# Performance work log

Hardware: AMD Instinct MI355X
Metric: run time of the kernel (lower is better)

Reference implementation:

```python
import jax, jax.numpy as jnp
import numpy as np

N_LEAVES = 8192   # perfect binary tree, depth 13
SEQ = 4096        # sequenceSize
EMB = 100         # embedSize
NCLS = 2          # numClasses


def setup_inputs() -> dict:
    key = jax.random.key(0)
    k = jax.random.split(key, 7)
    return {
        "leaf_seqs": jax.random.normal(k[0], (N_LEAVES, SEQ), dtype=jnp.float32),
        # torch nn.Linear stores weight as [out, in]; y = x @ W.T + b
        "We": jax.random.normal(k[1], (EMB, SEQ), dtype=jnp.float32) / np.sqrt(SEQ).astype(np.float32),
        "be": jax.random.normal(k[2], (EMB,), dtype=jnp.float32) * 0.01,
        "W": jax.random.normal(k[3], (EMB, 2 * EMB), dtype=jnp.float32) / np.sqrt(2 * EMB).astype(np.float32),
        "b": jax.random.normal(k[4], (EMB,), dtype=jnp.float32) * 0.01,
        "Wp": jax.random.normal(k[5], (NCLS, EMB), dtype=jnp.float32) / np.sqrt(EMB).astype(np.float32),
        "bp": jax.random.normal(k[6], (NCLS,), dtype=jnp.float32) * 0.01,
    }


def reference(leaf_seqs, We, be, W, b, Wp, bp):
    # Level-order (tree-batched) evaluation of the recursive RNN over a
    # perfect binary tree. Leaves: relu(embedding(seq)); internal nodes:
    # relu(W @ cat(left, right)); root: projection -> class logits.
    h = jax.nn.relu(leaf_seqs @ We.T + be)              # [n_leaves, emb]
    depth = int(np.log2(N_LEAVES))
    for _ in range(depth):                               # fixed small loop over levels
        # adjacent siblings: reshape gives cat((left, right), dim=1) per pair
        pairs = h.reshape(h.shape[0] // 2, 2 * h.shape[1])  # [n/2, 2*emb]
        h = jax.nn.relu(pairs @ W.T + b)                 # [n/2, emb]
    logits = h @ Wp.T + bp                               # [1, numClasses]
    return logits
```

## Files before the change

### kernel.cpp

```cpp
#include <hip/hip_runtime.h>


typedef _Float16 half_t;
typedef __attribute__((ext_vector_type(8))) _Float16 half8;
typedef __attribute__((ext_vector_type(4))) float floatx4;

#define VMCNT_4 0xF74
#define VMCNT_0 0xF70

__device__ __forceinline__ void gld_lds16(const float* g, float* l) {
  __builtin_amdgcn_global_load_lds((const __attribute__((address_space(1))) void*)g,
                                   (__attribute__((address_space(3))) void*)l, 16, 0, 0);
}

__device__ __forceinline__ void cvt_hilo(const floatx4& a, const floatx4& b, half8& hi, half8& lo) {
#pragma unroll
  for (int j = 0; j < 4; ++j) {
    float v = a[j];
    half_t hh = (half_t)v;
    hi[j] = hh; lo[j] = (half_t)(v - (float)hh);
  }
#pragma unroll
  for (int j = 0; j < 4; ++j) {
    float v = b[j];
    half_t hh = (half_t)v;
    hi[4 + j] = hh; lo[4 + j] = (half_t)(v - (float)hh);
  }
}

__global__ __launch_bounds__(256) void bprep(const float* __restrict__ We,
                                             half_t* __restrict__ Bf) {
  int t = blockIdx.x * 256 + threadIdx.x;
  if (t >= 51200) return;
  int n = t >> 9;
  int kp = t & 511;
  int k0 = kp * 8;
  int ks = k0 >> 5;
  int q = (k0 >> 3) & 3;
  int c = n >> 4, m = n & 15;
  int lane = q * 16 + m;

  const float* src = We + (size_t)n * 4096 + k0;
  half8 hv, lv;
#pragma unroll
  for (int j = 0; j < 8; ++j) {
    float w = src[j];
    half_t hh = (half_t)w;
    hv[j] = hh; lv[j] = (half_t)(w - (float)hh);
  }
  size_t base = (size_t)(ks * 14 + c * 2) * 64 + lane;
  *(half8*)(Bf + base * 8) = hv;
  *(half8*)(Bf + (base + 64) * 8) = lv;
}

__global__ __launch_bounds__(64) void wprep(const float* __restrict__ W,
                                            half_t* __restrict__ Wf) {
  int ks = blockIdx.x / 7, tt = blockIdx.x % 7;
  int lane = threadIdx.x;
  int q = lane >> 4, n = lane & 15;
  int col = tt * 16 + n;
  int kb = ks * 32 + q * 8;
  half8 hv, lv;
#pragma unroll
  for (int j = 0; j < 8; ++j) {
    int k = kb + j;
    float w = (col < 100 && k < 200) ? W[(size_t)col * 200 + k] : 0.f;
    half_t hh = (half_t)w;
    hv[j] = hh; lv[j] = (half_t)(w - (float)hh);
  }
  size_t base = (size_t)(ks * 14 + tt * 2) * 64 + lane;
  *(half8*)(Wf + base * 8) = hv;
  *(half8*)(Wf + (base + 64) * 8) = lv;
}

__global__ __launch_bounds__(512, 1) void leaf_mfma(const float* __restrict__ A,
                                                    const half8* __restrict__ Bf,
                                                    const float* __restrict__ be,
                                                    float* __restrict__ h0) {
  __shared__ __align__(16) float lds[3 * 8320];
  const int tid = threadIdx.x;
  const int lane = tid & 63;
  const int wave = tid >> 6;
  const int q = lane >> 4, m = lane & 15;
  const int r0 = blockIdx.x * 32;

  floatx4 acc[2][7];
#pragma unroll
  for (int t = 0; t < 2; ++t)
#pragma unroll
    for (int c = 0; c < 7; ++c) acc[t][c] = (floatx4){0.f, 0.f, 0.f, 0.f};

  const float* gbase = A + (size_t)(r0 + wave * 4) * 4096 + lane * 4;
  const int ldso = (wave * 4) * 260 + lane * 4;

  {
    const float* g0 = gbase;
    const float* g1 = gbase + 256;
#pragma unroll
    for (int i = 0; i < 4; ++i) gld_lds16(g0 + (size_t)i * 4096, lds + ldso + i * 260);
#pragma unroll
    for (int i = 0; i < 4; ++i) gld_lds16(g1 + (size_t)i * 4096, lds + 8320 + ldso + i * 260);
  }
  __builtin_amdgcn_s_waitcnt(VMCNT_4);
  __builtin_amdgcn_s_barrier();

  int bc = 0;
  for (int t = 0; t < 16; ++t) {
    const int ksg = t * 8 + wave;
    const half8* bb = Bf + (size_t)(ksg * 14) * 64 + lane;
    half8 bhi[7], blo[7];
#pragma unroll
    for (int c = 0; c < 7; ++c) { bhi[c] = bb[c * 128]; blo[c] = bb[c * 128 + 64]; }

    if (t < 14) {
      int bn = bc + 2; if (bn >= 3) bn -= 3;
      const float* g = gbase + (t + 2) * 256;
      float* d = lds + bn * 8320 + ldso;
#pragma unroll
      for (int i = 0; i < 4; ++i) gld_lds16(g + (size_t)i * 4096, d + i * 260);
    }

    const float* ap = lds + bc * 8320 + m * 260 + wave * 32 + q * 8;
    floatx4 a0 = *(const floatx4*)ap;
    floatx4 a1 = *(const floatx4*)(ap + 4);
    floatx4 a2 = *(const floatx4*)(ap + 16 * 260);
    floatx4 a3 = *(const floatx4*)(ap + 16 * 260 + 4);
    half8 ahi[2], alo[2];
    cvt_hilo(a0, a1, ahi[0], alo[0]);
    cvt_hilo(a2, a3, ahi[1], alo[1]);

#pragma unroll
    for (int c = 0; c < 7; ++c) {
      acc[0][c] = __builtin_amdgcn_mfma_f32_16x16x32_f16(ahi[0], bhi[c], acc[0][c], 0, 0, 0);
      acc[1][c] = __builtin_amdgcn_mfma_f32_16x16x32_f16(ahi[1], bhi[c], acc[1][c], 0, 0, 0);
      acc[0][c] = __builtin_amdgcn_mfma_f32_16x16x32_f16(alo[0], bhi[c], acc[0][c], 0, 0, 0);
      acc[1][c] = __builtin_amdgcn_mfma_f32_16x16x32_f16(alo[1], bhi[c], acc[1][c], 0, 0, 0);
      acc[0][c] = __builtin_amdgcn_mfma_f32_16x16x32_f16(ahi[0], blo[c], acc[0][c], 0, 0, 0);
      acc[1][c] = __builtin_amdgcn_mfma_f32_16x16x32_f16(ahi[1], blo[c], acc[1][c], 0, 0, 0);
    }

    if (t < 14) __builtin_amdgcn_s_waitcnt(VMCNT_4);
    else        __builtin_amdgcn_s_waitcnt(VMCNT_0);
    __builtin_amdgcn_s_barrier();

    bc += 1; if (bc >= 3) bc -= 3;
  }

  float* red = lds;
#pragma unroll
  for (int h = 4; h >= 1; h >>= 1) {
    if (wave >= h && wave < 2 * h) {
      float* d = red + (wave - h) * 3584;
#pragma unroll
      for (int t = 0; t < 2; ++t)
#pragma unroll
        for (int c = 0; c < 7; ++c)
#pragma unroll
          for (int r = 0; r < 4; ++r)
            d[(t * 16 + q * 4 + r) * 112 + c * 16 + m] = acc[t][c][r];
    }
    __syncthreads();
    if (wave < h) {
      const float* s = red + wave * 3584;
#pragma unroll
      for (int t = 0; t < 2; ++t)
#pragma unroll
        for (int c = 0; c < 7; ++c)
#pragma unroll
          for (int r = 0; r < 4; ++r)
            acc[t][c][r] += s[(t * 16 + q * 4 + r) * 112 + c * 16 + m];
    }
    __syncthreads();
  }

  if (wave == 0) {
#pragma unroll
    for (int c = 0; c < 7; ++c) {
      int col = c * 16 + m;
      if (col < 100) {
        float bv = be[col];
#pragma unroll
        for (int t = 0; t < 2; ++t)
#pragma unroll
          for (int r = 0; r < 4; ++r) {
            int row = r0 + t * 16 + q * 4 + r;
            h0[(size_t)row * 100 + col] = fmaxf(acc[t][c][r] + bv, 0.f);
          }
      }
    }
  }
}

template <int NVEC, bool PROJ>
__global__ __launch_bounds__(256, 1) void tree_mfma(const float* __restrict__ in,
                                                    float* __restrict__ out,
                                                    const half8* __restrict__ Wf,
                                                    const float* __restrict__ bt,
                                                    const float* __restrict__ Wp,
                                                    const float* __restrict__ bp) {
  __shared__ __align__(16) float bufA[16 * 228];
  __shared__ __align__(16) float bufB[16 * 228];
  const int tid = threadIdx.x;
  const int lane = tid & 63;
  const int wave = tid >> 6;
  const int q = lane >> 4, m = lane & 15;
  const int t0 = 2 * wave;
  const int t1 = (2 * wave + 1 > 6) ? 6 : 2 * wave + 1;

  half8 wh0[7], wl0[7], wh1[7], wl1[7];
#pragma unroll
  for (int ks = 0; ks < 7; ++ks) {
    wh0[ks] = Wf[(size_t)(ks * 14 + t0 * 2) * 64 + lane];
    wl0[ks] = Wf[(size_t)(ks * 14 + t0 * 2 + 1) * 64 + lane];
    wh1[ks] = Wf[(size_t)(ks * 14 + t1 * 2) * 64 + lane];
    wl1[ks] = Wf[(size_t)(ks * 14 + t1 * 2 + 1) * 64 + lane];
  }
  const int c0 = t0 * 16 + m;
  const int c1 = t1 * 16 + m;
  const float b0 = (c0 < 100) ? bt[c0] : 0.f;
  const float b1 = (c1 < 100) ? bt[c1] : 0.f;

  for (int i = tid; i < 16 * 228; i += 256) { bufA[i] = 0.f; bufB[i] = 0.f; }
  __syncthreads();
  const float* gin = in + (size_t)blockIdx.x * NVEC * 100;
  for (int i = tid; i < NVEC * 100; i += 256) {
    int v = i / 100, j = i - v * 100;
    bufA[(v >> 1) * 228 + (v & 1) * 100 + j] = gin[i];
  }
  __syncthreads();

  float* src = bufA;
  float* dst = bufB;
  constexpr int L = (NVEC == 32) ? 5 : 3;
#pragma unroll
  for (int l = 0; l < L; ++l) {
    const int nout = NVEC >> (l + 1);
    floatx4 acc0 = (floatx4){0.f, 0.f, 0.f, 0.f};
    floatx4 acc1 = (floatx4){0.f, 0.f, 0.f, 0.f};
#pragma unroll
    for (int ks = 0; ks < 7; ++ks) {
      const float* ap = src + m * 228 + ks * 32 + q * 8;
      floatx4 x0 = *(const floatx4*)ap;
      floatx4 x1 = *(const floatx4*)(ap + 4);
      half8 ah, al;
      cvt_hilo(x0, x1, ah, al);
      acc0 = __builtin_amdgcn_mfma_f32_16x16x32_f16(ah, wh0[ks], acc0, 0, 0, 0);
      acc1 = __builtin_amdgcn_mfma_f32_16x16x32_f16(ah, wh1[ks], acc1, 0, 0, 0);
      acc0 = __builtin_amdgcn_mfma_f32_16x16x32_f16(al, wh0[ks], acc0, 0, 0, 0);
      acc1 = __builtin_amdgcn_mfma_f32_16x16x32_f16(al, wh1[ks], acc1, 0, 0, 0);
      acc0 = __builtin_amdgcn_mfma_f32_16x16x32_f16(ah, wl0[ks], acc0, 0, 0, 0);
      acc1 = __builtin_amdgcn_mfma_f32_16x16x32_f16(ah, wl1[ks], acc1, 0, 0, 0);
    }
#pragma unroll
    for (int r = 0; r < 4; ++r) {
      int rowR = q * 4 + r;
      if (rowR < nout) {
        if (c0 < 100)
          dst[(rowR >> 1) * 228 + (rowR & 1) * 100 + c0] = fmaxf(acc0[r] + b0, 0.f);
        if (t1 != t0 && c1 < 100)
          dst[(rowR >> 1) * 228 + (rowR & 1) * 100 + c1] = fmaxf(acc1[r] + b1, 0.f);
      }
    }
    __syncthreads();
    float* tmp = src; src = dst; dst = tmp;
  }
  if (PROJ) {
    if (tid < 128) {
      int cls = tid >> 6, l = tid & 63;
      float sum = Wp[cls * 100 + l] * src[l];
      if (l + 64 < 100) sum += Wp[cls * 100 + l + 64] * src[l + 64];
#pragma unroll
      for (int off = 32; off > 0; off >>= 1) sum += __shfl_down(sum, off, 64);
      if (l == 0) out[cls] = sum + bp[cls];
    }
  } else {
    if (tid < 100) out[(size_t)blockIdx.x * 100 + tid] = src[tid];
  }
}

extern "C" void kernel_launch(void* const* d_in, const int* in_sizes, int n_in,
                              void* d_out, int out_size, void* d_ws, size_t ws_size,
                              hipStream_t stream) {
  (void)in_sizes; (void)n_in; (void)out_size; (void)ws_size;
  const float* leaf = (const float*)d_in[0];
  const float* We = (const float*)d_in[1];
  const float* be = (const float*)d_in[2];
  const float* W = (const float*)d_in[3];
  const float* b = (const float*)d_in[4];
  const float* Wp = (const float*)d_in[5];
  const float* bp = (const float*)d_in[6];
  float* out = (float*)d_out;

  char* ws = (char*)d_ws;
  half_t* Bf = (half_t*)ws;
  half_t* Wfr = (half_t*)(ws + 1835008);
  float* h0 = (float*)(ws + 1935360);
  float* h1 = (float*)(ws + 5212160);
  float* h2 = (float*)(ws + 5314560);

  bprep<<<dim3(200), dim3(256), 0, stream>>>(We, Bf);
  wprep<<<dim3(49), dim3(64), 0, stream>>>(W, Wfr);
  leaf_mfma<<<dim3(256), dim3(512), 0, stream>>>(leaf, (const half8*)Bf, be, h0);
  tree_mfma<32, false><<<dim3(256), dim3(256), 0, stream>>>(h0, h1, (const half8*)Wfr, b, nullptr, nullptr);
  tree_mfma<32, false><<<dim3(8), dim3(256), 0, stream>>>(h1, h2, (const half8*)Wfr, b, nullptr, nullptr);
  tree_mfma<8, true><<<dim3(1), dim3(256), 0, stream>>>(h2, out, (const half8*)Wfr, b, Wp, bp);
}
```

Measured before the change: 249.8 us.

## Split leaf GEMM over K halves, partition output columns across waves

The leaf GEMM kernel now splits K into two halves across separate blocks (512 blocks of 256 threads). Within a block, each wave owns a subset of output column tiles instead of a K slice, which removes the cross-wave LDS reduction. The two partial sums are written to a padded workspace and summed, with bias and ReLU, inside the first tree kernel's input load. The two weight-prep kernels are merged into one launch, and the leaf kernel moves from triple to double buffering. Each wave now rereads the full A tile from LDS for its columns, and the partial-sum output doubles the workspace traffic.

New measurement: 249.1 us. No clear change (-0.3%).

```diff
diff --git a/kernel.cpp b/kernel.cpp
--- a/kernel.cpp
+++ b/kernel.cpp
@@ -5,8 +5,7 @@
 typedef __attribute__((ext_vector_type(8))) _Float16 half8;
 typedef __attribute__((ext_vector_type(4))) float floatx4;
 
-#define VMCNT_4 0xF74
-#define VMCNT_0 0xF70
+#define H0ROWS ((size_t)8192 * 112)
 
 __device__ __forceinline__ void gld_lds16(const float* g, float* l) {
   __builtin_amdgcn_global_load_lds((const __attribute__((address_space(1))) void*)g,
@@ -28,174 +27,150 @@
   }
 }
 
-__global__ __launch_bounds__(256) void bprep(const float* __restrict__ We,
-                                             half_t* __restrict__ Bf) {
-  int t = blockIdx.x * 256 + threadIdx.x;
-  if (t >= 51200) return;
-  int n = t >> 9;
-  int kp = t & 511;
-  int k0 = kp * 8;
-  int ks = k0 >> 5;
-  int q = (k0 >> 3) & 3;
-  int c = n >> 4, m = n & 15;
-  int lane = q * 16 + m;
-
-  const float* src = We + (size_t)n * 4096 + k0;
-  half8 hv, lv;
-#pragma unroll
-  for (int j = 0; j < 8; ++j) {
-    float w = src[j];
-    half_t hh = (half_t)w;
-    hv[j] = hh; lv[j] = (half_t)(w - (float)hh);
-  }
-  size_t base = (size_t)(ks * 14 + c * 2) * 64 + lane;
-  *(half8*)(Bf + base * 8) = hv;
-  *(half8*)(Bf + (base + 64) * 8) = lv;
-}
-
-__global__ __launch_bounds__(64) void wprep(const float* __restrict__ W,
+__global__ __launch_bounds__(256) void prep(const float* __restrict__ We,
+                                            const float* __restrict__ W,
+                                            half_t* __restrict__ Bf,
                                             half_t* __restrict__ Wf) {
-  int ks = blockIdx.x / 7, tt = blockIdx.x % 7;
-  int lane = threadIdx.x;
-  int q = lane >> 4, n = lane & 15;
-  int col = tt * 16 + n;
-  int kb = ks * 32 + q * 8;
-  half8 hv, lv;
-#pragma unroll
-  for (int j = 0; j < 8; ++j) {
-    int k = kb + j;
-    float w = (col < 100 && k < 200) ? W[(size_t)col * 200 + k] : 0.f;
-    half_t hh = (half_t)w;
-    hv[j] = hh; lv[j] = (half_t)(w - (float)hh);
-  }
-  size_t base = (size_t)(ks * 14 + tt * 2) * 64 + lane;
-  *(half8*)(Wf + base * 8) = hv;
-  *(half8*)(Wf + (base + 64) * 8) = lv;
-}
-
-__global__ __launch_bounds__(512, 1) void leaf_mfma(const float* __restrict__ A,
+  if (blockIdx.x < 200) {
+    int t = blockIdx.x * 256 + threadIdx.x;
+    int n = t >> 9;
+    int kp = t & 511;
+    int k0 = kp * 8;
+    int ks = k0 >> 5;
+    int q = (k0 >> 3) & 3;
+    int c = n >> 4, m = n & 15;
+    int lane = q * 16 + m;
+    const float* src = We + (size_t)n * 4096 + k0;
+    half8 hv, lv;
+#pragma unroll
+    for (int j = 0; j < 8; ++j) {
+      float w = src[j];
+      half_t hh = (half_t)w;
+      hv[j] = hh; lv[j] = (half_t)(w - (float)hh);
+    }
+    size_t base = (size_t)(ks * 14 + c * 2) * 64 + lane;
+    *(half8*)(Bf + base * 8) = hv;
+    *(half8*)(Bf + (base + 64) * 8) = lv;
+  } else {
+    int u = (blockIdx.x - 200) * 256 + threadIdx.x;
+    if (u >= 3136) return;
+    int fb = u >> 6, lane = u & 63;
+    int ks = fb / 7, tt = fb % 7;
+    int q = lane >> 4, n = lane & 15;
+    int col = tt * 16 + n;
+    int kb = ks * 32 + q * 8;
+    half8 hv, lv;
+#pragma unroll
+    for (int j = 0; j < 8; ++j) {
+      int k = kb + j;
+      float w = (col < 100 && k < 200) ? W[(size_t)col * 200 + k] : 0.f;
+      half_t hh = (half_t)w;
+      hv[j] = hh; lv[j] = (half_t)(w - (float)hh);
+    }
+    size_t base = (size_t)(ks * 14 + tt * 2) * 64 + lane;
+    *(half8*)(Wf + base * 8) = hv;
+    *(half8*)(Wf + (base + 64) * 8) = lv;
+  }
+}
+
+__global__ __launch_bounds__(256, 2) void leaf_mfma(const float* __restrict__ A,
                                                     const half8* __restrict__ Bf,
-                                                    const float* __restrict__ be,
-                                                    float* __restrict__ h0) {
-  __shared__ __align__(16) float lds[3 * 8320];
+                                                    float* __restrict__ h0p) {
+  __shared__ __align__(16) float lds[2 * 8320];
   const int tid = threadIdx.x;
   const int lane = tid & 63;
   const int wave = tid >> 6;
   const int q = lane >> 4, m = lane & 15;
-  const int r0 = blockIdx.x * 32;
-
-  floatx4 acc[2][7];
-#pragma unroll
-  for (int t = 0; t < 2; ++t)
-#pragma unroll
-    for (int c = 0; c < 7; ++c) acc[t][c] = (floatx4){0.f, 0.f, 0.f, 0.f};
-
-  const float* gbase = A + (size_t)(r0 + wave * 4) * 4096 + lane * 4;
-  const int ldso = (wave * 4) * 260 + lane * 4;
-
-  {
-    const float* g0 = gbase;
-    const float* g1 = gbase + 256;
-#pragma unroll
-    for (int i = 0; i < 4; ++i) gld_lds16(g0 + (size_t)i * 4096, lds + ldso + i * 260);
-#pragma unroll
-    for (int i = 0; i < 4; ++i) gld_lds16(g1 + (size_t)i * 4096, lds + 8320 + ldso + i * 260);
-  }
-  __builtin_amdgcn_s_waitcnt(VMCNT_4);
-  __builtin_amdgcn_s_barrier();
-
-  int bc = 0;
-  for (int t = 0; t < 16; ++t) {
-    const int ksg = t * 8 + wave;
-    const half8* bb = Bf + (size_t)(ksg * 14) * 64 + lane;
-    half8 bhi[7], blo[7];
-#pragma unroll
-    for (int c = 0; c < 7; ++c) { bhi[c] = bb[c * 128]; blo[c] = bb[c * 128 + 64]; }
-
-    if (t < 14) {
-      int bn = bc + 2; if (bn >= 3) bn -= 3;
-      const float* g = gbase + (t + 2) * 256;
-      float* d = lds + bn * 8320 + ldso;
-#pragma unroll
-      for (int i = 0; i < 4; ++i) gld_lds16(g + (size_t)i * 4096, d + i * 260);
-    }
-
-    const float* ap = lds + bc * 8320 + m * 260 + wave * 32 + q * 8;
-    floatx4 a0 = *(const floatx4*)ap;
-    floatx4 a1 = *(const floatx4*)(ap + 4);
-    floatx4 a2 = *(const floatx4*)(ap + 16 * 260);
-    floatx4 a3 = *(const floatx4*)(ap + 16 * 260 + 4);
-    half8 ahi[2], alo[2];
-    cvt_hilo(a0, a1, ahi[0], alo[0]);
-    cvt_hilo(a2, a3, ahi[1], alo[1]);
-
-#pragma unroll
-    for (int c = 0; c < 7; ++c) {
-      acc[0][c] = __builtin_amdgcn_mfma_f32_16x16x32_f16(ahi[0], bhi[c], acc[0][c], 0, 0, 0);
-      acc[1][c] = __builtin_amdgcn_mfma_f32_16x16x32_f16(ahi[1], bhi[c], acc[1][c], 0, 0, 0);
-      acc[0][c] = __builtin_amdgcn_mfma_f32_16x16x32_f16(alo[0], bhi[c], acc[0][c], 0, 0, 0);
-      acc[1][c] = __builtin_amdgcn_mfma_f32_16x16x32_f16(alo[1], bhi[c], acc[1][c], 0, 0, 0);
-      acc[0][c] = __builtin_amdgcn_mfma_f32_16x16x32_f16(ahi[0], blo[c], acc[0][c], 0, 0, 0);
-      acc[1][c] = __builtin_amdgcn_mfma_f32_16x16x32_f16(ahi[1], blo[c], acc[1][c], 0, 0, 0);
-    }
-
-    if (t < 14) __builtin_amdgcn_s_waitcnt(VMCNT_4);
-    else        __builtin_amdgcn_s_waitcnt(VMCNT_0);
-    __builtin_amdgcn_s_barrier();
-
-    bc += 1; if (bc >= 3) bc -= 3;
-  }
-
-  float* red = lds;
-#pragma unroll
-  for (int h = 4; h >= 1; h >>= 1) {
-    if (wave >= h && wave < 2 * h) {
-      float* d = red + (wave - h) * 3584;
-#pragma unroll
-      for (int t = 0; t < 2; ++t)
-#pragma unroll
-        for (int c = 0; c < 7; ++c)
-#pragma unroll
-          for (int r = 0; r < 4; ++r)
-            d[(t * 16 + q * 4 + r) * 112 + c * 16 + m] = acc[t][c][r];
+  const int rt = blockIdx.x >> 1;
+  const int kh = blockIdx.x & 1;
+  const int r0 = rt * 32;
+  const int t0 = 2 * wave;
+  const int t1 = (2 * wave + 1 < 7) ? (2 * wave + 1) : 6;
+  const bool two = (t1 != t0);
+
+  floatx4 acc[2][2];
+#pragma unroll
+  for (int a = 0; a < 2; ++a)
+#pragma unroll
+    for (int c = 0; c < 2; ++c) acc[a][c] = (floatx4){0.f, 0.f, 0.f, 0.f};
+
+  const float* gbase = A + (size_t)(r0 + wave * 8) * 4096 + (size_t)kh * 2048 + lane * 4;
+  const int ldso = (wave * 8) * 260 + lane * 4;
+
+#pragma unroll
+  for (int i = 0; i < 8; ++i) gld_lds16(gbase + (size_t)i * 4096, lds + ldso + i * 260);
+  __syncthreads();
+
+  for (int t = 0; t < 8; ++t) {
+    half8 bh[8][2], bl[8][2];
+    const int ksgb = kh * 64 + t * 8;
+#pragma unroll
+    for (int k = 0; k < 8; ++k) {
+      const half8* bb = Bf + (size_t)((ksgb + k) * 14) * 64 + lane;
+      bh[k][0] = bb[(t0 * 2) * 64];
+      bl[k][0] = bb[(t0 * 2 + 1) * 64];
+      if (two) {
+        bh[k][1] = bb[(t1 * 2) * 64];
+        bl[k][1] = bb[(t1 * 2 + 1) * 64];
+      }
+    }
+    __builtin_amdgcn_sched_barrier(0);
+
+    if (t < 7) {
+      const float* g = gbase + (t + 1) * 256;
+      float* d = lds + ((t + 1) & 1) * 8320 + ldso;
+#pragma unroll
+      for (int i = 0; i < 8; ++i) gld_lds16(g + (size_t)i * 4096, d + i * 260);
+    }
+
+    const float* cur = lds + (t & 1) * 8320;
+#pragma unroll
+    for (int k = 0; k < 8; ++k) {
+      const float* ap = cur + m * 260 + k * 32 + q * 8;
+      floatx4 a0 = *(const floatx4*)ap;
+      floatx4 a1 = *(const floatx4*)(ap + 4);
+      floatx4 a2 = *(const floatx4*)(ap + 16 * 260);
+      floatx4 a3 = *(const floatx4*)(ap + 16 * 260 + 4);
+      half8 ah0, al0, ah1, al1;
+      cvt_hilo(a0, a1, ah0, al0);
+      cvt_hilo(a2, a3, ah1, al1);
+      acc[0][0] = __builtin_amdgcn_mfma_f32_16x16x32_f16(ah0, bh[k][0], acc[0][0], 0, 0, 0);
+      acc[1][0] = __builtin_amdgcn_mfma_f32_16x16x32_f16(ah1, bh[k][0], acc[1][0], 0, 0, 0);
+      acc[0][0] = __builtin_amdgcn_mfma_f32_16x16x32_f16(al0, bh[k][0], acc[0][0], 0, 0, 0);
+      acc[1][0] = __builtin_amdgcn_mfma_f32_16x16x32_f16(al1, bh[k][0], acc[1][0], 0, 0, 0);
+      acc[0][0] = __builtin_amdgcn_mfma_f32_16x16x32_f16(ah0, bl[k][0], acc[0][0], 0, 0, 0);
+      acc[1][0] = __builtin_amdgcn_mfma_f32_16x16x32_f16(ah1, bl[k][0], acc[1][0], 0, 0, 0);
+      if (two) {
+        acc[0][1] = __builtin_amdgcn_mfma_f32_16x16x32_f16(ah0, bh[k][1], acc[0][1], 0, 0, 0);
+        acc[1][1] = __builtin_amdgcn_mfma_f32_16x16x32_f16(ah1, bh[k][1], acc[1][1], 0, 0, 0);
+        acc[0][1] = __builtin_amdgcn_mfma_f32_16x16x32_f16(al0, bh[k][1], acc[0][1], 0, 0, 0);
+        acc[1][1] = __builtin_amdgcn_mfma_f32_16x16x32_f16(al1, bh[k][1], acc[1][1], 0, 0, 0);
+        acc[0][1] = __builtin_amdgcn_mfma_f32_16x16x32_f16(ah0, bl[k][1], acc[0][1], 0, 0, 0);
+        acc[1][1] = __builtin_amdgcn_mfma_f32_16x16x32_f16(ah1, bl[k][1], acc[1][1], 0, 0, 0);
+      }
     }
     __syncthreads();
-    if (wave < h) {
-      const float* s = red + wave * 3584;
-#pragma unroll
-      for (int t = 0; t < 2; ++t)
-#pragma unroll
-        for (int c = 0; c < 7; ++c)
-#pragma unroll
-          for (int r = 0; r < 4; ++r)
-            acc[t][c][r] += s[(t * 16 + q * 4 + r) * 112 + c * 16 + m];
-    }
-    __syncthreads();
-  }
-
-  if (wave == 0) {
-#pragma unroll
-    for (int c = 0; c < 7; ++c) {
-      int col = c * 16 + m;
-      if (col < 100) {
-        float bv = be[col];
-#pragma unroll
-        for (int t = 0; t < 2; ++t)
-#pragma unroll
-          for (int r = 0; r < 4; ++r) {
-            int row = r0 + t * 16 + q * 4 + r;
-            h0[(size_t)row * 100 + col] = fmaxf(acc[t][c][r] + bv, 0.f);
-          }
-      }
-    }
-  }
-}
-
-template <int NVEC, bool PROJ>
+  }
+
+  const size_t part = (size_t)kh * H0ROWS;
+#pragma unroll
+  for (int tt = 0; tt < 2; ++tt) {
+#pragma unroll
+    for (int r = 0; r < 4; ++r) {
+      int row = r0 + tt * 16 + q * 4 + r;
+      float* o = h0p + part + (size_t)row * 112;
+      o[t0 * 16 + m] = acc[tt][0][r];
+      if (two) o[t1 * 16 + m] = acc[tt][1][r];
+    }
+  }
+}
+
+template <int NVEC, bool PROJ, bool SUMIN>
 __global__ __launch_bounds__(256, 1) void tree_mfma(const float* __restrict__ in,
                                                     float* __restrict__ out,
                                                     const half8* __restrict__ Wf,
                                                     const float* __restrict__ bt,
+                                                    const float* __restrict__ be,
                                                     const float* __restrict__ Wp,
                                                     const float* __restrict__ bp) {
   __shared__ __align__(16) float bufA[16 * 228];
@@ -222,10 +197,19 @@
 
   for (int i = tid; i < 16 * 228; i += 256) { bufA[i] = 0.f; bufB[i] = 0.f; }
   __syncthreads();
-  const float* gin = in + (size_t)blockIdx.x * NVEC * 100;
-  for (int i = tid; i < NVEC * 100; i += 256) {
-    int v = i / 100, j = i - v * 100;
-    bufA[(v >> 1) * 228 + (v & 1) * 100 + j] = gin[i];
+  if (SUMIN) {
+    const size_t gb = (size_t)blockIdx.x * NVEC * 112;
+    for (int i = tid; i < NVEC * 100; i += 256) {
+      int v = i / 100, j = i - v * 100;
+      float x = fmaxf(in[gb + (size_t)v * 112 + j] + in[H0ROWS + gb + (size_t)v * 112 + j] + be[j], 0.f);
+      bufA[(v >> 1) * 228 + (v & 1) * 100 + j] = x;
+    }
+  } else {
+    const float* gin = in + (size_t)blockIdx.x * NVEC * 100;
+    for (int i = tid; i < NVEC * 100; i += 256) {
+      int v = i / 100, j = i - v * 100;
+      bufA[(v >> 1) * 228 + (v & 1) * 100 + j] = gin[i];
+    }
   }
   __syncthreads();
 
@@ -294,14 +278,13 @@
   char* ws = (char*)d_ws;
   half_t* Bf = (half_t*)ws;
   half_t* Wfr = (half_t*)(ws + 1835008);
-  float* h0 = (float*)(ws + 1935360);
-  float* h1 = (float*)(ws + 5212160);
-  float* h2 = (float*)(ws + 5314560);
-
-  bprep<<<dim3(200), dim3(256), 0, stream>>>(We, Bf);
-  wprep<<<dim3(49), dim3(64), 0, stream>>>(W, Wfr);
-  leaf_mfma<<<dim3(256), dim3(512), 0, stream>>>(leaf, (const half8*)Bf, be, h0);
-  tree_mfma<32, false><<<dim3(256), dim3(256), 0, stream>>>(h0, h1, (const half8*)Wfr, b, nullptr, nullptr);
-  tree_mfma<32, false><<<dim3(8), dim3(256), 0, stream>>>(h1, h2, (const half8*)Wfr, b, nullptr, nullptr);
-  tree_mfma<8, true><<<dim3(1), dim3(256), 0, stream>>>(h2, out, (const half8*)Wfr, b, Wp, bp);
-}
+  float* h0p = (float*)(ws + 1935360);
+  float* h1 = (float*)(ws + 9275392);
+  float* h2 = (float*)(ws + 9377792);
+
+  prep<<<dim3(213), dim3(256), 0, stream>>>(We, W, Bf, Wfr);
+  leaf_mfma<<<dim3(512), dim3(256), 0, stream>>>(leaf, (const half8*)Bf, h0p);
+  tree_mfma<32, false, true><<<dim3(256), dim3(256), 0, stream>>>(h0p, h1, (const half8*)Wfr, b, be, nullptr, nullptr);
+  tree_mfma<32, false, false><<<dim3(8), dim3(256), 0, stream>>>(h1, h2, (const half8*)Wfr, b, nullptr, nullptr, nullptr);
+  tree_mfma<8, true, false><<<dim3(1), dim3(256), 0, stream>>>(h2, out, (const half8*)Wfr, b, nullptr, Wp, bp);
+}
```
